# Performance work log

Hardware: AMD Instinct MI355X
Metric: run time of the kernel (lower is better)

## Reference

```python
import jax, jax.numpy as jnp
import numpy as np

N_ATOMS = 50000
N_EDGES = 800000
NODE_DIM = 64
EDGE_DIM = 64
FULL_DIM = 2 * NODE_DIM + EDGE_DIM
BN_EPS = 1e-5


def setup_inputs() -> dict:
    key = jax.random.key(0)
    ks = jax.random.split(key, 8)
    atom_features = jax.random.normal(ks[0], (N_ATOMS, NODE_DIM), dtype=jnp.float32)
    edge_features = jax.random.normal(ks[1], (N_EDGES, EDGE_DIM), dtype=jnp.float32)
    edge_indices = jax.random.randint(ks[2], (N_EDGES, 2), 0, N_ATOMS, dtype=jnp.int64)
    lim = 1.0 / np.sqrt(FULL_DIM)
    W_filter = jax.random.uniform(ks[3], (NODE_DIM, FULL_DIM), jnp.float32, -lim, lim)
    b_filter = jax.random.uniform(ks[4], (NODE_DIM,), jnp.float32, -lim, lim)
    W_core = jax.random.uniform(ks[5], (NODE_DIM, FULL_DIM), jnp.float32, -lim, lim)
    b_core = jax.random.uniform(ks[6], (NODE_DIM,), jnp.float32, -lim, lim)
    gamma_filter = jnp.ones((NODE_DIM,), jnp.float32)
    beta_filter = jnp.zeros((NODE_DIM,), jnp.float32)
    gamma_core = jnp.ones((NODE_DIM,), jnp.float32)
    beta_core = jnp.zeros((NODE_DIM,), jnp.float32)
    return {
        "atom_features": atom_features,
        "edge_features": edge_features,
        "W_filter": W_filter, "b_filter": b_filter,
        "gamma_filter": gamma_filter, "beta_filter": beta_filter,
        "W_core": W_core, "b_core": b_core,
        "gamma_core": gamma_core, "beta_core": beta_core,
        "edge_indices": edge_indices,
    }


def _batchnorm(x, gamma, beta):
    # training-mode BN over the edge axis (biased variance, as torch uses for normalization)
    mean = jnp.mean(x, axis=0)
    var = jnp.mean(jnp.square(x - mean), axis=0)
    return (x - mean) * jax.lax.rsqrt(var + BN_EPS) * gamma + beta


def reference(atom_features, edge_features, W_filter, b_filter, gamma_filter,
              beta_filter, W_core, b_core, gamma_core, beta_core, edge_indices):
    src = edge_indices[:, 0]
    dst = edge_indices[:, 1]
    # z_ij: [E, 2*node_dim + edge_dim]
    z = jnp.concatenate([atom_features[dst], atom_features[src], edge_features], axis=1)
    signal = jax.nn.softplus(_batchnorm(z @ W_core.T + b_core, gamma_core, beta_core))
    gate = jax.nn.sigmoid(_batchnorm(z @ W_filter.T + b_filter, gamma_filter, beta_filter))
    message = gate * signal  # [E, node_dim]
    nbr_sumed = jax.ops.segment_sum(message, dst, num_segments=atom_features.shape[0])
    return atom_features + nbr_sumed
```

## Files before the change

kernel.cpp:

```cpp
#include <hip/hip_runtime.h>
#include <hip/hip_bf16.h>
#include <math.h>

#define N_ATOMS   50000
#define N_EDGES   800000
#define KDIM      192
#define BN_EPS    1e-5f

#define TILE_E     64
#define TPB        5
#define NTILES     (N_EDGES / TILE_E)
#define GRID1      (NTILES / TPB)
#define STAT_SLOTS 32
#define ZSTRIDE    200

typedef __attribute__((ext_vector_type(8))) __bf16 bf16x8;
typedef __attribute__((ext_vector_type(4))) float  f32x4;
typedef __attribute__((ext_vector_type(4))) unsigned short u16x4;

__device__ __forceinline__ ushort f2bf(float f) {
    union { float f; unsigned u; } v; v.f = f;
    unsigned u = v.u;
    return (ushort)((u + 0x7FFFu + ((u >> 16) & 1u)) >> 16);
}
__device__ __forceinline__ float bf2f(unsigned hi16) {
    union { unsigned u; float f; } v; v.u = hi16 << 16; return v.f;
}

__device__ __forceinline__ void gather_tile(
    const float* __restrict__ atom, const float* __restrict__ edgef,
    const int* eidxl, int tilebase, ushort* zl, int tid)
{
    const int er = tid >> 4, f4 = tid & 15;
    const float* p[12];
#pragma unroll
    for (int it = 0; it < 12; ++it) {
        const int seg = it >> 2;
        const int e   = (it & 3) * 16 + er;
        const float* srcp;
        if (seg == 0)      srcp = atom  + (size_t)eidxl[2 * e + 1] * 64;
        else if (seg == 1) srcp = atom  + (size_t)eidxl[2 * e] * 64;
        else               srcp = edgef + (size_t)(tilebase + e) * 64;
        p[it] = srcp + f4 * 4;
    }
    f32x4 v[12];
#pragma unroll
    for (int it = 0; it < 12; ++it) {
        if ((it >> 2) == 2) v[it] = __builtin_nontemporal_load((const f32x4*)p[it]);
        else                v[it] = *(const f32x4*)p[it];
    }
#pragma unroll
    for (int it = 0; it < 12; ++it) {
        const int seg = it >> 2;
        const int e   = (it & 3) * 16 + er;
        u16x4 b;
        b.x = f2bf(v[it].x); b.y = f2bf(v[it].y);
        b.z = f2bf(v[it].z); b.w = f2bf(v[it].w);
        *(u16x4*)&zl[e * ZSTRIDE + seg * 64 + f4 * 4] = b;
    }
}

__global__ __launch_bounds__(256) void gemm_stats_store(
    const float* __restrict__ atom, const float* __restrict__ edgef,
    const ushort* __restrict__ Wb, const int* __restrict__ eidx,
    float* __restrict__ stat_partial, unsigned* __restrict__ ws_pre,
    int do_store)
{
    __shared__ __align__(16) ushort zl[TILE_E * ZSTRIDE];
    __shared__ int eidxl[TPB * 128];
    const int tid  = threadIdx.x;
    const int lane = tid & 63, wave = tid >> 6;
    const int ch = wave >> 1, rp = wave & 1;
    const int row = lane & 15, quad = lane >> 4;

    const int base2 = blockIdx.x * TPB * 128;
    for (int i = tid; i < TPB * 128; i += 256) eidxl[i] = eidx[base2 + i];

    bf16x8 bfr[2][2][6];
#pragma unroll
    for (int m = 0; m < 2; ++m)
#pragma unroll
        for (int nt = 0; nt < 2; ++nt)
#pragma unroll
            for (int ks = 0; ks < 6; ++ks)
                bfr[m][nt][ks] = *(const bf16x8*)&Wb[
                    (size_t)(m * 64 + ch * 32 + nt * 16 + row) * KDIM + ks * 32 + quad * 8];

    float s[2][2] = {{0.f, 0.f}, {0.f, 0.f}};
    float q[2][2] = {{0.f, 0.f}, {0.f, 0.f}};

    const int t0 = blockIdx.x * TPB;
    for (int tt = 0; tt < TPB; ++tt) {
        const int tilebase = (t0 + tt) * TILE_E;
        __syncthreads();
        gather_tile(atom, edgef, eidxl + tt * 128, tilebase, zl, tid);
        __syncthreads();
#pragma unroll
        for (int ett = 0; ett < 2; ++ett) {
            const ushort* zb = zl + ((2 * rp + ett) * 16 + row) * ZSTRIDE;
            bf16x8 a[6];
#pragma unroll
            for (int ks = 0; ks < 6; ++ks)
                a[ks] = *(const bf16x8*)&zb[ks * 32 + quad * 8];
            f32x4 acc[2][2];
#pragma unroll
            for (int m = 0; m < 2; ++m)
#pragma unroll
                for (int nt = 0; nt < 2; ++nt)
                    acc[m][nt] = (f32x4){0.f, 0.f, 0.f, 0.f};
#pragma unroll
            for (int ks = 0; ks < 6; ++ks)
#pragma unroll
                for (int m = 0; m < 2; ++m)
#pragma unroll
                    for (int nt = 0; nt < 2; ++nt)
                        acc[m][nt] = __builtin_amdgcn_mfma_f32_16x16x32_bf16(
                            a[ks], bfr[m][nt][ks], acc[m][nt], 0, 0, 0);
#pragma unroll
            for (int nt = 0; nt < 2; ++nt) {
                const int c = ch * 32 + nt * 16 + row;
#pragma unroll
                for (int r = 0; r < 4; ++r) {
                    float vc = acc[0][nt][r], vf = acc[1][nt][r];
                    s[0][nt] += vc; q[0][nt] += vc * vc;
                    s[1][nt] += vf; q[1][nt] += vf * vf;
                    if (do_store) {
                        const int eloc = (2 * rp + ett) * 16 + quad * 4 + r;
                        unsigned pack = (unsigned)f2bf(vc) | ((unsigned)f2bf(vf) << 16);
                        __builtin_nontemporal_store(pack,
                            ws_pre + (size_t)(tilebase + eloc) * 64 + c);
                    }
                }
            }
        }
    }

    float* slot = stat_partial + (size_t)(blockIdx.x & (STAT_SLOTS - 1)) * 256;
#pragma unroll
    for (int m = 0; m < 2; ++m)
#pragma unroll
        for (int nt = 0; nt < 2; ++nt) {
            float sv = s[m][nt], qv = q[m][nt];
            sv += __shfl_xor(sv, 16, 64); sv += __shfl_xor(sv, 32, 64);
            qv += __shfl_xor(qv, 16, 64); qv += __shfl_xor(qv, 32, 64);
            if (lane < 16) {
                int c = ch * 32 + nt * 16 + lane;
                atomicAdd(slot + m * 128 + c, sv);
                atomicAdd(slot + m * 128 + 64 + c, qv);
            }
        }
}

__global__ void finalize_stats(const float* __restrict__ stat_partial,
                               const float* __restrict__ gc, const float* __restrict__ btc,
                               const float* __restrict__ gf, const float* __restrict__ btf,
                               float* __restrict__ params)
{
    int t = threadIdx.x;
    bool isf = t >= 64;
    int j = t & 63;
    float s = 0.f, q = 0.f;
    for (int slot = 0; slot < STAT_SLOTS; slot++) {
        const float* sp = stat_partial + (size_t)slot * 256 + (isf ? 128 : 0);
        s += sp[j];
        q += sp[64 + j];
    }
    float mean = s / (float)N_EDGES;
    float var  = q / (float)N_EDGES - mean * mean;
    float inv  = rsqrtf(var + BN_EPS);
    float gamma = isf ? gf[j] : gc[j];
    float beta  = isf ? btf[j] : btc[j];
    float scale = gamma * inv;
    float shift = beta - mean * scale;
    params[t]       = scale;
    params[128 + t] = shift;
}

__global__ __launch_bounds__(256) void copy_out(const f32x4* __restrict__ src,
                                                f32x4* __restrict__ dst)
{
    int i = blockIdx.x * blockDim.x + threadIdx.x;
    dst[i] = src[i];
}

__global__ __launch_bounds__(256) void convert_weights(
    const float* __restrict__ Wc, const float* __restrict__ Wf,
    ushort* __restrict__ Wb)
{
    int i = blockIdx.x * 256 + threadIdx.x;
    float v = (i < 64 * KDIM) ? Wc[i] : Wf[i - 64 * KDIM];
    Wb[i] = f2bf(v);
}

__global__ __launch_bounds__(256) void bn_act_scatter(
    const unsigned* __restrict__ ws_pre, const int* __restrict__ eidx,
    const float* __restrict__ params, float* __restrict__ out)
{
    const int lane = threadIdx.x & 63;
    const int gw   = blockIdx.x * 4 + (threadIdx.x >> 6);
    const int e0   = gw * 64;

    const float sc_c = params[lane],      sh_c = params[128 + lane];
    const float sc_f = params[64 + lane], sh_f = params[192 + lane];

    for (int i = 0; i < 64; i += 8) {
        unsigned pv[8]; int dv[8];
#pragma unroll
        for (int k = 0; k < 8; ++k) {
            int e = e0 + i + k;
            pv[k] = __builtin_nontemporal_load(ws_pre + (size_t)e * 64 + lane);
            dv[k] = eidx[2 * e + 1];
        }
#pragma unroll
        for (int k = 0; k < 8; ++k) {
            float pc = fmaf(bf2f(pv[k] & 0xFFFFu), sc_c, sh_c);
            float pf = fmaf(bf2f(pv[k] >> 16),     sc_f, sh_f);
            float sp = fmaxf(pc, 0.f) + __logf(1.f + __expf(-fabsf(pc)));
            float sg = 1.f / (1.f + __expf(-pf));
            atomicAdd(out + (size_t)dv[k] * 64 + lane, sp * sg);
        }
    }
}

__global__ __launch_bounds__(256) void apply_scatter_fb(
    const float* __restrict__ atom, const float* __restrict__ edgef,
    const ushort* __restrict__ Wb, const int* __restrict__ eidx,
    const float* __restrict__ params, float* __restrict__ out)
{
    __shared__ __align__(16) ushort zl[TILE_E * ZSTRIDE];
    __shared__ int eidxl[TPB * 128];
    const int tid  = threadIdx.x;
    const int lane = tid & 63, wave = tid >> 6;
    const int ch = wave >> 1, rp = wave & 1;
    const int row = lane & 15, quad = lane >> 4;

    const int base2 = blockIdx.x * TPB * 128;
    for (int i = tid; i < TPB * 128; i += 256) eidxl[i] = eidx[base2 + i];

    bf16x8 bfr[2][2][6];
#pragma unroll
    for (int m = 0; m < 2; ++m)
#pragma unroll
        for (int nt = 0; nt < 2; ++nt)
#pragma unroll
            for (int ks = 0; ks < 6; ++ks)
                bfr[m][nt][ks] = *(const bf16x8*)&Wb[
                    (size_t)(m * 64 + ch * 32 + nt * 16 + row) * KDIM + ks * 32 + quad * 8];

    float scc[2], shc[2], scf[2], shf[2];
#pragma unroll
    for (int nt = 0; nt < 2; ++nt) {
        int c = ch * 32 + nt * 16 + row;
        scc[nt] = params[c];        shc[nt] = params[128 + c];
        scf[nt] = params[64 + c];   shf[nt] = params[192 + c];
    }

    const int t0 = blockIdx.x * TPB;
    for (int tt = 0; tt < TPB; ++tt) {
        const int tilebase = (t0 + tt) * TILE_E;
        __syncthreads();
        gather_tile(atom, edgef, eidxl + tt * 128, tilebase, zl, tid);
        __syncthreads();
#pragma unroll
        for (int ett = 0; ett < 2; ++ett) {
            const ushort* zb = zl + ((2 * rp + ett) * 16 + row) * ZSTRIDE;
            bf16x8 a[6];
#pragma unroll
            for (int ks = 0; ks < 6; ++ks)
                a[ks] = *(const bf16x8*)&zb[ks * 32 + quad * 8];
            f32x4 acc[2][2];
#pragma unroll
            for (int m = 0; m < 2; ++m)
#pragma unroll
                for (int nt = 0; nt < 2; ++nt)
                    acc[m][nt] = (f32x4){0.f, 0.f, 0.f, 0.f};
#pragma unroll
            for (int ks = 0; ks < 6; ++ks)
#pragma unroll
                for (int m = 0; m < 2; ++m)
#pragma unroll
                    for (int nt = 0; nt < 2; ++nt)
                        acc[m][nt] = __builtin_amdgcn_mfma_f32_16x16x32_bf16(
                            a[ks], bfr[m][nt][ks], acc[m][nt], 0, 0, 0);
#pragma unroll
            for (int nt = 0; nt < 2; ++nt) {
                int c = ch * 32 + nt * 16 + row;
#pragma unroll
                for (int r = 0; r < 4; ++r) {
                    float pc = fmaf(acc[0][nt][r], scc[nt], shc[nt]);
                    float pf = fmaf(acc[1][nt][r], scf[nt], shf[nt]);
                    float sp = fmaxf(pc, 0.f) + __logf(1.f + __expf(-fabsf(pc)));
                    float sg = 1.f / (1.f + __expf(-pf));
                    int eloc = (2 * rp + ett) * 16 + quad * 4 + r;
                    int d = eidxl[tt * 128 + 2 * eloc + 1];
                    atomicAdd(out + (size_t)d * 64 + c, sp * sg);
                }
            }
        }
    }
}

extern "C" void kernel_launch(void* const* d_in, const int* in_sizes, int n_in,
                              void* d_out, int out_size, void* d_ws, size_t ws_size,
                              hipStream_t stream)
{
    const float* atom  = (const float*)d_in[0];
    const float* edgef = (const float*)d_in[1];
    const float* Wf    = (const float*)d_in[2];
    const float* gf    = (const float*)d_in[4];
    const float* btf   = (const float*)d_in[5];
    const float* Wc    = (const float*)d_in[6];
    const float* gc    = (const float*)d_in[8];
    const float* btc   = (const float*)d_in[9];
    const int*   eidx  = (const int*)d_in[10];
    float* out = (float*)d_out;

    float*    stat_partial = (float*)d_ws;
    float*    params       = stat_partial + STAT_SLOTS * 256;
    ushort*   Wb           = (ushort*)(params + 256);
    unsigned* ws_pre       = (unsigned*)(Wb + 2 * 64 * KDIM);

    const size_t need = (size_t)STAT_SLOTS * 256 * 4 + 256 * 4 +
                        (size_t)2 * 64 * KDIM * 2 + (size_t)N_EDGES * 64 * 4;
    const int cache = (ws_size >= need) ? 1 : 0;

    (void)hipMemsetAsync(d_ws, 0, STAT_SLOTS * 256 * sizeof(float), stream);
    convert_weights<<<(2 * 64 * KDIM) / 256, 256, 0, stream>>>(Wc, Wf, Wb);

    gemm_stats_store<<<GRID1, 256, 0, stream>>>(atom, edgef, Wb, eidx,
                                                stat_partial, ws_pre, cache);
    finalize_stats<<<1, 128, 0, stream>>>(stat_partial, gc, btc, gf, btf, params);
    copy_out<<<(N_ATOMS * 64 / 4) / 256, 256, 0, stream>>>(
        (const f32x4*)atom, (f32x4*)out);
    if (cache)
        bn_act_scatter<<<N_EDGES / (4 * 64), 256, 0, stream>>>(ws_pre, eidx,
                                                               params, out);
    else
        apply_scatter_fb<<<GRID1, 256, 0, stream>>>(atom, edgef, Wb, eidx,
                                                    params, out);
}
```

Measured before the change: 568.6 us.

## Replace atomic scatter with per-atom CSR gather reduction

```diff
diff --git a/kernel.cpp b/kernel.cpp
--- a/kernel.cpp
+++ b/kernel.cpp
@@ -13,6 +13,7 @@
 #define GRID1      (NTILES / TPB)
 #define STAT_SLOTS 32
 #define ZSTRIDE    200
+#define NSCANBLK   ((N_ATOMS + 255) / 256)
 
 typedef __attribute__((ext_vector_type(8))) __bf16 bf16x8;
 typedef __attribute__((ext_vector_type(4))) float  f32x4;
@@ -25,6 +26,14 @@
 }
 __device__ __forceinline__ float bf2f(unsigned hi16) {
     union { unsigned u; float f; } v; v.u = hi16 << 16; return v.f;
+}
+__device__ __forceinline__ float msgf(unsigned pv, float sc_c, float sh_c,
+                                      float sc_f, float sh_f) {
+    float pc = fmaf(bf2f(pv & 0xFFFFu), sc_c, sh_c);
+    float pf = fmaf(bf2f(pv >> 16),     sc_f, sh_f);
+    float sp = fmaxf(pc, 0.f) + __logf(1.f + __expf(-fabsf(pc)));
+    float sg = 1.f / (1.f + __expf(-pf));
+    return sp * sg;
 }
 
 __device__ __forceinline__ void gather_tile(
@@ -176,13 +185,6 @@
     params[128 + t] = shift;
 }
 
-__global__ __launch_bounds__(256) void copy_out(const f32x4* __restrict__ src,
-                                                f32x4* __restrict__ dst)
-{
-    int i = blockIdx.x * blockDim.x + threadIdx.x;
-    dst[i] = src[i];
-}
-
 __global__ __launch_bounds__(256) void convert_weights(
     const float* __restrict__ Wc, const float* __restrict__ Wf,
     ushort* __restrict__ Wb)
@@ -192,34 +194,110 @@
     Wb[i] = f2bf(v);
 }
 
-__global__ __launch_bounds__(256) void bn_act_scatter(
-    const unsigned* __restrict__ ws_pre, const int* __restrict__ eidx,
+__global__ __launch_bounds__(256) void hist_dst(const int* __restrict__ eidx,
+                                                unsigned* __restrict__ counts)
+{
+    int e = blockIdx.x * 256 + threadIdx.x;
+    atomicAdd(&counts[eidx[2 * e + 1]], 1u);
+}
+
+__global__ __launch_bounds__(256) void scan_a(const unsigned* __restrict__ counts,
+                                              unsigned* __restrict__ row_start,
+                                              unsigned* __restrict__ blksum)
+{
+    __shared__ unsigned sh[256];
+    const int tid = threadIdx.x;
+    const int i = blockIdx.x * 256 + tid;
+    unsigned v = (i < N_ATOMS) ? counts[i] : 0u;
+    sh[tid] = v;
+    __syncthreads();
+    for (int off = 1; off < 256; off <<= 1) {
+        unsigned t = (tid >= off) ? sh[tid - off] : 0u;
+        __syncthreads();
+        sh[tid] += t;
+        __syncthreads();
+    }
+    if (i < N_ATOMS) row_start[i] = sh[tid] - v;
+    if (tid == 255) blksum[blockIdx.x] = sh[tid];
+}
+
+__global__ void scan_b(unsigned* __restrict__ blksum)
+{
+    __shared__ unsigned sh[256];
+    const int tid = threadIdx.x;
+    unsigned v = (tid < NSCANBLK) ? blksum[tid] : 0u;
+    sh[tid] = v;
+    __syncthreads();
+    for (int off = 1; off < 256; off <<= 1) {
+        unsigned t = (tid >= off) ? sh[tid - off] : 0u;
+        __syncthreads();
+        sh[tid] += t;
+        __syncthreads();
+    }
+    if (tid < NSCANBLK) blksum[tid] = sh[tid] - v;
+}
+
+__global__ __launch_bounds__(256) void init_cursor(unsigned* __restrict__ row_start,
+                                                   const unsigned* __restrict__ blksum,
+                                                   unsigned* __restrict__ cursors)
+{
+    int i = blockIdx.x * 256 + threadIdx.x;
+    if (i < N_ATOMS) {
+        unsigned base = row_start[i] + blksum[i >> 8];
+        row_start[i] = base;
+        cursors[i]   = base;
+    }
+    if (i == 0) row_start[N_ATOMS] = N_EDGES;
+}
+
+__global__ __launch_bounds__(256) void fill_csr(const int* __restrict__ eidx,
+                                                unsigned* __restrict__ cursors,
+                                                unsigned* __restrict__ csr)
+{
+    int e = blockIdx.x * 256 + threadIdx.x;
+    int d = eidx[2 * e + 1];
+    unsigned pos = atomicAdd(&cursors[d], 1u);
+    csr[pos] = (unsigned)e;
+}
+
+__global__ __launch_bounds__(256) void bn_act_reduce(
+    const unsigned* __restrict__ ws_pre, const unsigned* __restrict__ csr,
+    const unsigned* __restrict__ row_start, const float* __restrict__ atom,
     const float* __restrict__ params, float* __restrict__ out)
 {
     const int lane = threadIdx.x & 63;
-    const int gw   = blockIdx.x * 4 + (threadIdx.x >> 6);
-    const int e0   = gw * 64;
+    const int a    = blockIdx.x * 4 + (threadIdx.x >> 6);
 
     const float sc_c = params[lane],      sh_c = params[128 + lane];
     const float sc_f = params[64 + lane], sh_f = params[192 + lane];
 
-    for (int i = 0; i < 64; i += 8) {
-        unsigned pv[8]; int dv[8];
-#pragma unroll
-        for (int k = 0; k < 8; ++k) {
-            int e = e0 + i + k;
-            pv[k] = __builtin_nontemporal_load(ws_pre + (size_t)e * 64 + lane);
-            dv[k] = eidx[2 * e + 1];
-        }
-#pragma unroll
-        for (int k = 0; k < 8; ++k) {
-            float pc = fmaf(bf2f(pv[k] & 0xFFFFu), sc_c, sh_c);
-            float pf = fmaf(bf2f(pv[k] >> 16),     sc_f, sh_f);
-            float sp = fmaxf(pc, 0.f) + __logf(1.f + __expf(-fabsf(pc)));
-            float sg = 1.f / (1.f + __expf(-pf));
-            atomicAdd(out + (size_t)dv[k] * 64 + lane, sp * sg);
-        }
-    }
+    unsigned j   = row_start[a];
+    unsigned end = row_start[a + 1];
+    float acc = 0.f;
+
+    for (; j + 4 <= end; j += 4) {
+        unsigned e0 = csr[j], e1 = csr[j + 1], e2 = csr[j + 2], e3 = csr[j + 3];
+        unsigned p0 = ws_pre[(size_t)e0 * 64 + lane];
+        unsigned p1 = ws_pre[(size_t)e1 * 64 + lane];
+        unsigned p2 = ws_pre[(size_t)e2 * 64 + lane];
+        unsigned p3 = ws_pre[(size_t)e3 * 64 + lane];
+        acc += msgf(p0, sc_c, sh_c, sc_f, sh_f);
+        acc += msgf(p1, sc_c, sh_c, sc_f, sh_f);
+        acc += msgf(p2, sc_c, sh_c, sc_f, sh_f);
+        acc += msgf(p3, sc_c, sh_c, sc_f, sh_f);
+    }
+    for (; j < end; ++j) {
+        unsigned e = csr[j];
+        acc += msgf(ws_pre[(size_t)e * 64 + lane], sc_c, sh_c, sc_f, sh_f);
+    }
+    out[(size_t)a * 64 + lane] = atom[(size_t)a * 64 + lane] + acc;
+}
+
+__global__ __launch_bounds__(256) void copy_out(const f32x4* __restrict__ src,
+                                                f32x4* __restrict__ dst)
+{
+    int i = blockIdx.x * blockDim.x + threadIdx.x;
+    dst[i] = src[i];
 }
 
 __global__ __launch_bounds__(256) void apply_scatter_fb(
@@ -315,27 +393,41 @@
     const int*   eidx  = (const int*)d_in[10];
     float* out = (float*)d_out;
 
-    float*    stat_partial = (float*)d_ws;
+    unsigned* ws_pre       = (unsigned*)d_ws;
+    float*    stat_partial = (float*)(ws_pre + (size_t)N_EDGES * 64);
     float*    params       = stat_partial + STAT_SLOTS * 256;
     ushort*   Wb           = (ushort*)(params + 256);
-    unsigned* ws_pre       = (unsigned*)(Wb + 2 * 64 * KDIM);
-
-    const size_t need = (size_t)STAT_SLOTS * 256 * 4 + 256 * 4 +
-                        (size_t)2 * 64 * KDIM * 2 + (size_t)N_EDGES * 64 * 4;
-    const int cache = (ws_size >= need) ? 1 : 0;
-
-    (void)hipMemsetAsync(d_ws, 0, STAT_SLOTS * 256 * sizeof(float), stream);
+    unsigned* counts       = (unsigned*)(Wb + 2 * 64 * KDIM);
+    unsigned* row_start    = counts + N_ATOMS;
+    unsigned* blksum       = row_start + N_ATOMS + 1;
+    unsigned* cursors      = blksum + 256;
+    unsigned* csr          = cursors + N_ATOMS;
+
+    const size_t need_full = (size_t)((char*)(csr + N_EDGES) - (char*)d_ws);
+    const int full = (ws_size >= need_full) ? 1 : 0;
+
+    (void)hipMemsetAsync(stat_partial, 0, STAT_SLOTS * 256 * sizeof(float), stream);
     convert_weights<<<(2 * 64 * KDIM) / 256, 256, 0, stream>>>(Wc, Wf, Wb);
 
-    gemm_stats_store<<<GRID1, 256, 0, stream>>>(atom, edgef, Wb, eidx,
-                                                stat_partial, ws_pre, cache);
-    finalize_stats<<<1, 128, 0, stream>>>(stat_partial, gc, btc, gf, btf, params);
-    copy_out<<<(N_ATOMS * 64 / 4) / 256, 256, 0, stream>>>(
-        (const f32x4*)atom, (f32x4*)out);
-    if (cache)
-        bn_act_scatter<<<N_EDGES / (4 * 64), 256, 0, stream>>>(ws_pre, eidx,
-                                                               params, out);
-    else
+    if (full) {
+        (void)hipMemsetAsync(counts, 0, N_ATOMS * sizeof(unsigned), stream);
+        hist_dst<<<N_EDGES / 256, 256, 0, stream>>>(eidx, counts);
+        gemm_stats_store<<<GRID1, 256, 0, stream>>>(atom, edgef, Wb, eidx,
+                                                    stat_partial, ws_pre, 1);
+        finalize_stats<<<1, 128, 0, stream>>>(stat_partial, gc, btc, gf, btf, params);
+        scan_a<<<NSCANBLK, 256, 0, stream>>>(counts, row_start, blksum);
+        scan_b<<<1, 256, 0, stream>>>(blksum);
+        init_cursor<<<NSCANBLK, 256, 0, stream>>>(row_start, blksum, cursors);
+        fill_csr<<<N_EDGES / 256, 256, 0, stream>>>(eidx, cursors, csr);
+        bn_act_reduce<<<N_ATOMS / 4, 256, 0, stream>>>(ws_pre, csr, row_start,
+                                                       atom, params, out);
+    } else {
+        gemm_stats_store<<<GRID1, 256, 0, stream>>>(atom, edgef, Wb, eidx,
+                                                    stat_partial, ws_pre, 0);
+        finalize_stats<<<1, 128, 0, stream>>>(stat_partial, gc, btc, gf, btf, params);
+        copy_out<<<(N_ATOMS * 64 / 4) / 256, 256, 0, stream>>>(
+            (const f32x4*)atom, (f32x4*)out);
         apply_scatter_fb<<<GRID1, 256, 0, stream>>>(atom, edgef, Wb, eidx,
                                                     params, out);
-}
+    }
+}
```

After: 555.1 us. -2.4%, faster.
